# Kernel optimization log

Measured on AMD Instinct MI355X. Metric: run time of the kernel, lower is better.

Reference implementation:

```python
import jax, jax.numpy as jnp
import numpy as np

H = 2048   # hidden_size
E = 4096   # intermediate_size
N = 16     # ssm_state_size
K = 4      # conv_kernel
R = 128    # time_step_rank
B_SZ = 2
L = 2048


def setup_inputs() -> dict:
    key = jax.random.key(0)
    ks = jax.random.split(key, 9)
    s = lambda fan: 1.0 / np.sqrt(fan)
    hidden_states = jax.random.normal(ks[0], (B_SZ, L, H), dtype=jnp.float32)
    in_proj_w = jax.random.normal(ks[1], (2 * E, H), dtype=jnp.float32) * s(H)
    conv_w = jax.random.normal(ks[2], (E, 1, K), dtype=jnp.float32) * s(K)
    conv_b = jax.random.normal(ks[3], (E,), dtype=jnp.float32) * 0.01
    x_proj_w = jax.random.normal(ks[4], (R + 2 * N, E), dtype=jnp.float32) * s(E)
    dt_proj_w = jax.random.normal(ks[5], (E, R), dtype=jnp.float32) * s(R)
    dt_proj_b = jax.random.normal(ks[6], (E,), dtype=jnp.float32) * 0.01
    A_log = jnp.log(jnp.broadcast_to(jnp.arange(1, N + 1, dtype=jnp.float32)[None, :], (E, N)))
    D = jnp.ones((E,), dtype=jnp.float32)
    out_proj_w = jax.random.normal(ks[7], (H, E), dtype=jnp.float32) * s(E)
    return {
        "hidden_states": hidden_states,
        "in_proj_w": in_proj_w,
        "conv_w": conv_w,
        "conv_b": conv_b,
        "x_proj_w": x_proj_w,
        "dt_proj_w": dt_proj_w,
        "dt_proj_b": dt_proj_b,
        "A_log": A_log,
        "D": D,
        "out_proj_w": out_proj_w,
    }


def _mamba_fwd(hidden_states, in_proj_w, conv_w, conv_b, x_proj_w,
               dt_proj_w, dt_proj_b, A_log, D, out_proj_w):
    # in_proj -> [B, L, 2E] -> transpose -> [B, 2E, L] -> chunk
    proj = jnp.einsum('blh,eh->ble', hidden_states, in_proj_w)
    proj = jnp.transpose(proj, (0, 2, 1))              # [B, 2E, L]
    u, gate = jnp.split(proj, 2, axis=1)               # each [B, E, L]

    # causal depthwise conv1d (pad K-1 left), then silu
    x = jax.lax.conv_general_dilated(
        u, conv_w, window_strides=(1,), padding=[(K - 1, 0)],
        dimension_numbers=('NCH', 'OIH', 'NCH'), feature_group_count=E)
    x = jax.nn.silu(x + conv_b[None, :, None])          # [B, E, L]

    # x_proj -> dt, B, C
    x_bl = jnp.transpose(x, (0, 2, 1))                  # [B, L, E]
    x_dbl = jnp.einsum('ble,re->blr', x_bl, x_proj_w)   # [B, L, R+2N]
    dt_low, Bmat, Cmat = jnp.split(x_dbl, [R, R + N], axis=-1)
    dt = jax.nn.softplus(jnp.einsum('blr,er->ble', dt_low, dt_proj_w) + dt_proj_b)  # [B, L, E]

    A = -jnp.exp(A_log)                                 # [E, N]

    # selective scan over time; carry state [B, E, N]
    def step(s, inp):
        dt_t, u_t, B_t, C_t = inp                       # [B,E],[B,E],[B,N],[B,N]
        dA = jnp.exp(dt_t[..., None] * A[None])         # [B, E, N]
        s = s * dA + (dt_t * u_t)[..., None] * B_t[:, None, :]
        y_t = jnp.einsum('ben,bn->be', s, C_t)
        return s, y_t

    xs = (jnp.transpose(dt, (1, 0, 2)),                 # [L, B, E]
          jnp.transpose(x, (2, 0, 1)),                  # [L, B, E]
          jnp.transpose(Bmat, (1, 0, 2)),               # [L, B, N]
          jnp.transpose(Cmat, (1, 0, 2)))               # [L, B, N]
    s0 = jnp.zeros((hidden_states.shape[0], E, N), dtype=jnp.float32)
    _, ys = jax.lax.scan(step, s0, xs)                  # ys: [L, B, E]

    y = jnp.transpose(ys, (1, 2, 0))                    # [B, E, L]
    y = y + x * D[None, :, None]
    y = y * jax.nn.silu(gate)
    out = jnp.einsum('bel,he->blh', y, out_proj_w)      # [B, L, H]
    return out


def reference(hidden_states, in_proj_w, conv_w, conv_b, x_proj_w,
              dt_proj_w, dt_proj_b, A_log, D, out_proj_w):
    return _mamba_fwd(hidden_states, in_proj_w, conv_w, conv_b, x_proj_w,
                      dt_proj_w, dt_proj_b, A_log, D, out_proj_w)
```

## Files before the change

kernel.cpp:

```cpp
#include <hip/hip_runtime.h>
#include <math.h>

#define Hd 2048
#define Ed 4096
#define Nssm 16
#define Rrank 128
#define Bb 2
#define Ll 2048
#define Mrows (Bb*Ll)
#define XDBL_C 160
#define Cc 64
#define Tc (Ll/Cc)

typedef unsigned short u16;
typedef short bf16x8 __attribute__((ext_vector_type(8)));
typedef float f32x4 __attribute__((ext_vector_type(4)));
typedef u16 us4 __attribute__((ext_vector_type(4)));
typedef u16 us8 __attribute__((ext_vector_type(8)));

__device__ __forceinline__ u16 f2bf(float f) {
    unsigned u = __float_as_uint(f);
    u += 0x7FFFu + ((u >> 16) & 1u);
    return (u16)(u >> 16);
}
__device__ __forceinline__ float bf2f(u16 h) {
    return __uint_as_float((unsigned)h << 16);
}
__device__ __forceinline__ float fexp(float x)  { return __expf(x); }
__device__ __forceinline__ float fsig(float x)  { return __builtin_amdgcn_rcpf(1.f + __expf(-x)); }
__device__ __forceinline__ float fsoftplus(float z) {
    return fmaxf(z, 0.f) + __logf(1.f + __expf(-fabsf(z)));
}

__device__ __forceinline__ void stage_tile(const char* g, int ldbytes, char* lds, int tid)
{
#pragma unroll
    for (int q = 0; q < 4; ++q) {
        int idx = q * 256 + tid;
        int row = idx >> 3;
        int cb  = (idx & 7) << 4;
        int sb  = cb ^ ((row & 7) << 4);
        __builtin_amdgcn_global_load_lds(
            (const __attribute__((address_space(1))) void*)(g + (size_t)row * ldbytes + sb),
            (__attribute__((address_space(3))) void*)(lds + (size_t)idx * 16),
            16, 0, 0);
    }
}

__device__ __forceinline__ void stage_half(const char* g, int ldbytes, char* lds, int tid)
{
#pragma unroll
    for (int q = 0; q < 2; ++q) {
        int idx = q * 512 + tid;
        int row = idx >> 3;
        int cb  = (idx & 7) << 4;
        int sb  = cb ^ ((row & 7) << 4);
        __builtin_amdgcn_global_load_lds(
            (const __attribute__((address_space(1))) void*)(g + (size_t)row * ldbytes + sb),
            (__attribute__((address_space(3))) void*)(lds + (size_t)idx * 16),
            16, 0, 0);
    }
}

template<int NKT, int CBF16>
__global__ __launch_bounds__(512, 2)
void gemm_3buf(const u16* __restrict__ A, const u16* __restrict__ Bw,
               void* __restrict__ Cp, int ld, int ldc)
{
    __shared__ __align__(16) char lds[147456];
    const int tid = threadIdx.x;
    const int bm = blockIdx.y * 256;
    const int bn = blockIdx.x * 128;
    const int lane = tid & 63;
    const int wv = tid >> 6;
    const int wm = wv >> 1;
    const int wn = wv & 1;
    const int lr = lane & 15, kg = lane >> 4;

    f32x4 acc[4][4];
#pragma unroll
    for (int f = 0; f < 4; ++f)
#pragma unroll
        for (int g = 0; g < 4; ++g) acc[f][g] = (f32x4){0.f, 0.f, 0.f, 0.f};

    bf16x8 av[4][2], bv[2][2];

#define BUFA(b) (lds + (b) * 49152)
#define BUFB(b) (lds + (b) * 49152 + 32768)
#define STAGE_A3(t, b) { \
    stage_half((const char*)A + ((size_t)(bm)       * ld + (t)*64) * 2, ld*2, BUFA(b), tid); \
    stage_half((const char*)A + ((size_t)(bm + 128) * ld + (t)*64) * 2, ld*2, BUFA(b) + 16384, tid); }
#define STAGE_B3(t, b) \
    stage_half((const char*)Bw + ((size_t)(bn)      * ld + (t)*64) * 2, ld*2, BUFB(b), tid)
#define READ_A3(b) { const char* p_ = BUFA(b); \
    _Pragma("unroll") for (int f = 0; f < 4; ++f) { \
        int row = wm*64 + f*16 + lr; int sw = (row & 7) << 4; \
        const char* rb = p_ + row * 128; \
        av[f][0] = *(const bf16x8*)(rb + ((kg*16) ^ sw)); \
        av[f][1] = *(const bf16x8*)(rb + ((64 + kg*16) ^ sw)); } }
#define READ_B3(b, u) { const char* p_ = BUFB(b); \
    _Pragma("unroll") for (int g = 0; g < 2; ++g) { \
        int row = wn*64 + (u)*32 + g*16 + lr; int sw = (row & 7) << 4; \
        const char* rb = p_ + row * 128; \
        bv[g][0] = *(const bf16x8*)(rb + ((kg*16) ^ sw)); \
        bv[g][1] = *(const bf16x8*)(rb + ((64 + kg*16) ^ sw)); } }
#define QUAD3(u) { \
    _Pragma("unroll") for (int f = 0; f < 4; ++f) \
    _Pragma("unroll") for (int g = 0; g < 2; ++g) { \
        acc[f][(u)*2+g] = __builtin_amdgcn_mfma_f32_16x16x32_bf16(av[f][0], bv[g][0], acc[f][(u)*2+g], 0, 0, 0); \
        acc[f][(u)*2+g] = __builtin_amdgcn_mfma_f32_16x16x32_bf16(av[f][1], bv[g][1], acc[f][(u)*2+g], 0, 0, 0); } }
#define BAR __builtin_amdgcn_s_barrier()
#define VMW(n) { asm volatile("s_waitcnt vmcnt(" #n ")" ::: "memory"); __builtin_amdgcn_sched_barrier(0); }

    STAGE_A3(0, 0); STAGE_B3(0, 0);
    STAGE_A3(1, 1); STAGE_B3(1, 1);
    VMW(6);
    BAR;

    int bc = 0;
    for (int t = 0; t < NKT; ++t) {
        int b2 = bc + 2; if (b2 >= 3) b2 -= 3;
        READ_A3(bc); READ_B3(bc, 0);
        if (t + 2 < NKT) STAGE_A3(t + 2, b2);
        BAR; __builtin_amdgcn_s_setprio(1); QUAD3(0); __builtin_amdgcn_s_setprio(0); BAR;
        READ_B3(bc, 1);
        if (t + 2 < NKT) STAGE_B3(t + 2, b2);
        BAR; __builtin_amdgcn_s_setprio(1); QUAD3(1); __builtin_amdgcn_s_setprio(0);
        if (t + 2 < NKT) { VMW(6); } else if (t + 1 < NKT) { VMW(0); }
        BAR;
        bc = (bc + 1 == 3) ? 0 : bc + 1;
    }

#pragma unroll
    for (int f = 0; f < 4; ++f) {
        int rbase = bm + wm * 64 + f * 16 + kg * 4;
#pragma unroll
        for (int g = 0; g < 4; ++g) {
            int col = bn + wn * 64 + g * 16 + lr;
#pragma unroll
            for (int r = 0; r < 4; ++r) {
                float v = acc[f][g][r];
                if (CBF16) ((u16*)Cp)[(size_t)(rbase + r) * ldc + col] = f2bf(v);
                else       ((float*)Cp)[(size_t)(rbase + r) * ldc + col] = v;
            }
        }
    }
#undef BUFA
#undef BUFB
#undef STAGE_A3
#undef STAGE_B3
#undef READ_A3
#undef READ_B3
#undef QUAD3
#undef BAR
#undef VMW
}

template<int EPI, int CBF16>
__global__ __launch_bounds__(256)
void gemm_bf16(const u16* __restrict__ A, const u16* __restrict__ Bw,
               void* __restrict__ Cp, const float* __restrict__ bias,
               int Nv, int Ksub, int lda, int ldb, int ldc, size_t zstride)
{
    __shared__ __align__(16) char lds[32768];
    char* ldsA = lds;
    char* ldsB = lds + 16384;
    const int tid = threadIdx.x;
    const int bm = blockIdx.y * 128;
    const int bn = blockIdx.x * 128;
    const int lane = tid & 63, wv = tid >> 6;
    const int wr = (wv >> 1) * 64, wc = (wv & 1) * 64;
    const int lr = lane & 15, kg = lane >> 4;
    const int kbeg = blockIdx.z * Ksub;

    f32x4 acc[4][4];
#pragma unroll
    for (int m = 0; m < 4; ++m)
#pragma unroll
        for (int n = 0; n < 4; ++n) acc[m][n] = (f32x4){0.f, 0.f, 0.f, 0.f};

    for (int k0 = kbeg; k0 < kbeg + Ksub; k0 += 64) {
        stage_tile((const char*)A  + ((size_t)bm * lda + k0) * 2, lda * 2, ldsA, tid);
        stage_tile((const char*)Bw + ((size_t)bn * ldb + k0) * 2, ldb * 2, ldsB, tid);
        __syncthreads();
#pragma unroll
        for (int kk = 0; kk < 2; ++kk) {
            const int bc = kk * 64 + kg * 16;
            bf16x8 bfr[4], af[4];
#pragma unroll
            for (int n = 0; n < 4; ++n) {
                int row = wc + n * 16 + lr;
                bfr[n] = *(const bf16x8*)(ldsB + row * 128 + (bc ^ ((row & 7) << 4)));
            }
#pragma unroll
            for (int m = 0; m < 4; ++m) {
                int row = wr + m * 16 + lr;
                af[m] = *(const bf16x8*)(ldsA + row * 128 + (bc ^ ((row & 7) << 4)));
            }
#pragma unroll
            for (int m = 0; m < 4; ++m)
#pragma unroll
                for (int n = 0; n < 4; ++n)
                    acc[m][n] = __builtin_amdgcn_mfma_f32_16x16x32_bf16(af[m], bfr[n], acc[m][n], 0, 0, 0);
        }
        __syncthreads();
    }

    if (zstride) Cp = (void*)((float*)Cp + (size_t)blockIdx.z * zstride);

#pragma unroll
    for (int m = 0; m < 4; ++m) {
        int rbase = bm + wr + m * 16 + kg * 4;
#pragma unroll
        for (int n = 0; n < 4; ++n) {
            int col = bn + wc + n * 16 + lr;
            if (col < Nv) {
#pragma unroll
                for (int r = 0; r < 4; ++r) {
                    float v = acc[m][n][r];
                    if (EPI == 1) v = fsoftplus(v + bias[col]);
                    if (CBF16) ((u16*)Cp)[(size_t)(rbase + r) * ldc + col] = f2bf(v);
                    else       ((float*)Cp)[(size_t)(rbase + r) * ldc + col] = v;
                }
            }
        }
    }
}

__global__ __launch_bounds__(256)
void reduce_cast(const float* __restrict__ part, float* __restrict__ outf,
                 u16* __restrict__ outb, int cnt, size_t stride, int total)
{
    int i = blockIdx.x * 256 + threadIdx.x;
    if (i < total) {
        float v = 0.f;
        for (int z = 0; z < cnt; z++) v += part[(size_t)z * stride + i];
        outf[i] = v;
        outb[i] = f2bf(v);
    }
}

__global__ __launch_bounds__(256)
void cast_w(const float* __restrict__ s, u16* __restrict__ d, int n)
{
    int i = (blockIdx.x * 256 + threadIdx.x) * 8;
    if (i >= n) return;
    float4 a = *(const float4*)(s + i);
    float4 b = *(const float4*)(s + i + 4);
    us8 o;
    o[0] = f2bf(a.x); o[1] = f2bf(a.y); o[2] = f2bf(a.z); o[3] = f2bf(a.w);
    o[4] = f2bf(b.x); o[5] = f2bf(b.y); o[6] = f2bf(b.z); o[7] = f2bf(b.w);
    *(us8*)(d + i) = o;
}

__global__ __launch_bounds__(256)
void cast_wx(const float* __restrict__ s, u16* __restrict__ d)
{
    int i4 = (blockIdx.x * 256 + threadIdx.x) * 4;
    int row = i4 >> 12;
    us4 o = (us4){0, 0, 0, 0};
    if (row < XDBL_C) {
        float4 v = *(const float4*)(s + i4);
        o[0] = f2bf(v.x); o[1] = f2bf(v.y); o[2] = f2bf(v.z); o[3] = f2bf(v.w);
    }
    *(us4*)(d + i4) = o;
}

__global__ __launch_bounds__(256)
void conv_silu_bf(const u16* __restrict__ proj, const float* __restrict__ cw,
                  const float* __restrict__ cb, u16* __restrict__ x)
{
    const int e  = blockIdx.x * 256 + threadIdx.x;
    const int t0 = blockIdx.y * 32;
    const int bz = blockIdx.z;
    const float4 w4 = *(const float4*)(cw + (size_t)e * 4);
    const float bias = cb[e];
    const size_t base = (size_t)bz * Ll * (2 * Ed) + e;

    float u0 = 0.f, u1 = 0.f, u2 = 0.f;
    if (t0 >= 3) {
        u0 = bf2f(proj[base + (size_t)(t0 - 3) * (2 * Ed)]);
        u1 = bf2f(proj[base + (size_t)(t0 - 2) * (2 * Ed)]);
        u2 = bf2f(proj[base + (size_t)(t0 - 1) * (2 * Ed)]);
    }
    size_t xo = ((size_t)(bz * Ll + t0)) * Ed + e;
#pragma unroll 4
    for (int t = t0; t < t0 + 32; ++t) {
        float u3 = bf2f(proj[base + (size_t)t * (2 * Ed)]);
        float acc = bias;
        acc = fmaf(w4.x, u0, acc);
        acc = fmaf(w4.y, u1, acc);
        acc = fmaf(w4.z, u2, acc);
        acc = fmaf(w4.w, u3, acc);
        float sx = acc * fsig(acc);
        x[xo] = f2bf(sx);
        xo += Ed;
        u0 = u1; u1 = u2; u2 = u3;
    }
}

__global__ __launch_bounds__(256)
void scan_part1(const u16* __restrict__ proj, const u16* __restrict__ x,
                const float* __restrict__ xdbl, const float* __restrict__ Alog,
                float* __restrict__ S, float* __restrict__ sumdt)
{
    const int e = blockIdx.x * 256 + threadIdx.x;
    const int c = blockIdx.y;
    const int b = blockIdx.z;

    float Ae[Nssm];
#pragma unroll
    for (int n = 0; n < Nssm; n++) Ae[n] = -fexp(Alog[(size_t)e * Nssm + n]);

    float s[Nssm];
#pragma unroll
    for (int n = 0; n < Nssm; n++) s[n] = 0.f;
    float sdt = 0.f;

    const size_t row0 = (size_t)b * Ll + (size_t)c * Tc;
    for (int t = 0; t < Tc; ++t) {
        size_t r = row0 + t;
        float dtv = bf2f(proj[r * (2 * Ed) + e]);
        float uv  = bf2f(x[r * Ed + e]);
        const float* p = xdbl + r * XDBL_C + Rrank;
        float du = dtv * uv;
        sdt += dtv;
#pragma unroll
        for (int n = 0; n < Nssm; n++)
            s[n] = fmaf(s[n], fexp(dtv * Ae[n]), du * p[n]);
    }

    float* sp = S + ((((size_t)b * Cc + c) * Ed + e) * Nssm);
#pragma unroll
    for (int n = 0; n < Nssm; n += 4)
        *(float4*)(sp + n) = make_float4(s[n], s[n+1], s[n+2], s[n+3]);
    sumdt[((size_t)b * Cc + c) * Ed + e] = sdt;
}

__global__ __launch_bounds__(256)
void scan_mid(float* __restrict__ S, const float* __restrict__ sumdt,
              const float* __restrict__ Alog)
{
    const int idx = blockIdx.x * 256 + threadIdx.x;
    const int n = idx & (Nssm - 1);
    const int e = (idx >> 4) & (Ed - 1);
    const int b = idx >> 16;
    const float Ae = -fexp(Alog[(size_t)e * Nssm + n]);
    float carry = 0.f;
    for (int c = 0; c < Cc; ++c) {
        size_t off = (((size_t)b * Cc + c) * Ed + e) * Nssm + n;
        float sl = S[off];
        float P  = fexp(Ae * sumdt[((size_t)b * Cc + c) * Ed + e]);
        S[off] = carry;
        carry = fmaf(P, carry, sl);
    }
}

__global__ __launch_bounds__(256)
void scan_part2(const u16* __restrict__ proj, u16* __restrict__ x,
                const float* __restrict__ xdbl, const float* __restrict__ Alog,
                const float* __restrict__ Dvec, const float* __restrict__ S)
{
    const int e = blockIdx.x * 256 + threadIdx.x;
    const int c = blockIdx.y;
    const int b = blockIdx.z;

    float Ae[Nssm];
#pragma unroll
    for (int n = 0; n < Nssm; n++) Ae[n] = -fexp(Alog[(size_t)e * Nssm + n]);
    const float Dv = Dvec[e];

    float s[Nssm];
    const float* sp = S + ((((size_t)b * Cc + c) * Ed + e) * Nssm);
#pragma unroll
    for (int n = 0; n < Nssm; n += 4) {
        float4 v = *(const float4*)(sp + n);
        s[n] = v.x; s[n+1] = v.y; s[n+2] = v.z; s[n+3] = v.w;
    }

    const size_t row0 = (size_t)b * Ll + (size_t)c * Tc;
    for (int t = 0; t < Tc; ++t) {
        size_t r = row0 + t;
        float dtv = bf2f(proj[r * (2 * Ed) + e]);
        float uv  = bf2f(x[r * Ed + e]);
        float gv  = bf2f(proj[r * (2 * Ed) + Ed + e]);
        const float* p = xdbl + r * XDBL_C + Rrank;
        float du = dtv * uv;
        float y = 0.f;
#pragma unroll
        for (int n = 0; n < Nssm; n++) {
            float dA = fexp(dtv * Ae[n]);
            s[n] = fmaf(s[n], dA, du * p[n]);
            y = fmaf(s[n], p[Nssm + n], y);
        }
        float yv = (y + uv * Dv) * (gv * fsig(gv));
        x[r * Ed + e] = f2bf(yv);
    }
}

extern "C" void kernel_launch(void* const* d_in, const int* in_sizes, int n_in,
                              void* d_out, int out_size, void* d_ws, size_t ws_size,
                              hipStream_t stream) {
    const float* hs    = (const float*)d_in[0];
    const float* w_in  = (const float*)d_in[1];
    const float* cw    = (const float*)d_in[2];
    const float* cb    = (const float*)d_in[3];
    const float* w_x   = (const float*)d_in[4];
    const float* w_dt  = (const float*)d_in[5];
    const float* b_dt  = (const float*)d_in[6];
    const float* Alog  = (const float*)d_in[7];
    const float* Dvec  = (const float*)d_in[8];
    const float* w_out = (const float*)d_in[9];
    float* out = (float*)d_out;

    char* w = (char*)d_ws;
    u16*  proj_bf  = (u16*)w;
    u16*  x_bf     = (u16*)(w + 67108864);
    u16*  w_in_bf  = (u16*)(w + 100663296);
    u16*  w_out_bf = (u16*)(w + 134217728);
    u16*  hs_bf    = (u16*)(w + 150994944);
    u16*  w_x_bf   = (u16*)(w + 167772160);
    u16*  w_dt_bf  = (u16*)(w + 169869312);
    float* xdbl    = (float*)(w + 170917888);
    u16*  xdbl_bf  = (u16*)(w + 173539328);
    float* part    = (float*)(w + 174850048);
    float* sumdt   = (float*)(w + 185335808);
    float* S       = (float*)(w + 187432960);

    dim3 blk(256);

    cast_w<<<dim3(8192), blk, 0, stream>>>(w_in, w_in_bf, 2 * Ed * Hd);
    cast_w<<<dim3(4096), blk, 0, stream>>>(w_out, w_out_bf, Hd * Ed);
    cast_w<<<dim3(256),  blk, 0, stream>>>(w_dt, w_dt_bf, Ed * Rrank);
    cast_wx<<<dim3(1024), blk, 0, stream>>>(w_x, w_x_bf);
    cast_w<<<dim3(4096), blk, 0, stream>>>(hs, hs_bf, Mrows * Hd);

    gemm_3buf<Hd / 64, 1><<<dim3(2 * Ed / 128, Mrows / 256), dim3(512), 0, stream>>>(
        hs_bf, w_in_bf, proj_bf, Hd, 2 * Ed);

    conv_silu_bf<<<dim3(Ed / 256, Ll / 32, Bb), blk, 0, stream>>>(proj_bf, cw, cb, x_bf);

    gemm_bf16<0, 0><<<dim3(2, 32, 4), blk, 0, stream>>>(
        x_bf, w_x_bf, part, nullptr, XDBL_C, Ed / 4, Ed, Ed, XDBL_C,
        (size_t)Mrows * XDBL_C);
    reduce_cast<<<dim3((Mrows * XDBL_C + 255) / 256), blk, 0, stream>>>(
        part, xdbl, xdbl_bf, 4, (size_t)Mrows * XDBL_C, Mrows * XDBL_C);

    gemm_bf16<1, 1><<<dim3(32, 32, 1), blk, 0, stream>>>(
        xdbl_bf, w_dt_bf, proj_bf, b_dt, Ed, Rrank, XDBL_C, Rrank, 2 * Ed, 0);

    scan_part1<<<dim3(Ed / 256, Cc, Bb), blk, 0, stream>>>(
        proj_bf, x_bf, xdbl, Alog, S, sumdt);
    scan_mid<<<dim3(Bb * Ed * Nssm / 256), blk, 0, stream>>>(S, sumdt, Alog);
    scan_part2<<<dim3(Ed / 256, Cc, Bb), blk, 0, stream>>>(
        proj_bf, x_bf, xdbl, Alog, Dvec, S);

    gemm_3buf<Ed / 64, 0><<<dim3(Hd / 128, Mrows / 256), dim3(512), 0, stream>>>(
        x_bf, w_out_bf, out, Ed, Hd);
}
```

Measured before the change: 418.9 us.

## Replace in_proj GEMM with 256x256-tile eight-phase pipelined kernel

Swaps the 256x128-tile triple-buffered in_proj GEMM for a new 256x256-tile kernel. It double-buffers A and B half-tiles in LDS and interleaves half-tile global-to-LDS loads with MFMA quadrants over eight barrier-separated phases, raising wave priority around the MFMA bursts. The larger tile increases operand reuse per block and halves the grid in N. In exchange it holds more accumulator registers per thread and adds many barriers with hand-tuned vmcnt waits that must match the load order exactly.

```diff
diff --git a/kernel.cpp b/kernel.cpp
--- a/kernel.cpp
+++ b/kernel.cpp
@@ -60,6 +60,118 @@
             (__attribute__((address_space(3))) void*)(lds + (size_t)idx * 16),
             16, 0, 0);
     }
+}
+
+#define NK8  32
+#define NI8  16
+
+__global__ __launch_bounds__(512, 2)
+void gemm_8ph_inproj(const u16* __restrict__ A, const u16* __restrict__ Bw,
+                     u16* __restrict__ C)
+{
+    __shared__ __align__(16) char lds[131072];
+    const int tid = threadIdx.x;
+    const int bm = blockIdx.y * 256;
+    const int bn = blockIdx.x * 256;
+    const int lane = tid & 63;
+    const int wv = tid >> 6;
+    const int wm = wv >> 2;
+    const int wn = wv & 3;
+    const int lr = lane & 15, kg = lane >> 4;
+
+    f32x4 acc[8][4];
+#pragma unroll
+    for (int m = 0; m < 8; ++m)
+#pragma unroll
+        for (int n = 0; n < 4; ++n) acc[m][n] = (f32x4){0.f, 0.f, 0.f, 0.f};
+
+    bf16x8 av[4][2], bv0[2][2], bv1[2][2];
+
+#define ASLOT(d, h) (lds + ((d)*2 + (h)) * 16384)
+#define BSLOT(d, h) (lds + 65536 + ((d)*2 + (h)) * 16384)
+#define STAGE_AH(t, h) stage_half((const char*)A  + ((size_t)(bm + (h)*128) * Hd + (t)*64) * 2, Hd*2, ASLOT((t)&1, h), tid)
+#define STAGE_BH(t, h) stage_half((const char*)Bw + ((size_t)(bn + (h)*128) * Hd + (t)*64) * 2, Hd*2, BSLOT((t)&1, h), tid)
+
+#define READ_A(d, s) { \
+    const char* slot_ = ASLOT(d, wm); \
+    _Pragma("unroll") for (int f = 0; f < 4; ++f) { \
+        int row = (s)*64 + f*16 + lr; int sw = (row & 7) << 4; \
+        const char* rb = slot_ + row * 128; \
+        av[f][0] = *(const bf16x8*)(rb + ((kg*16) ^ sw)); \
+        av[f][1] = *(const bf16x8*)(rb + ((64 + kg*16) ^ sw)); } }
+#define READ_B(d, u, bvX) { \
+    const char* slot_ = BSLOT(d, (wn >> 1)); \
+    _Pragma("unroll") for (int g2 = 0; g2 < 2; ++g2) { \
+        int row = (wn & 1)*64 + (u)*32 + g2*16 + lr; int sw = (row & 7) << 4; \
+        const char* rb = slot_ + row * 128; \
+        bvX[g2][0] = *(const bf16x8*)(rb + ((kg*16) ^ sw)); \
+        bvX[g2][1] = *(const bf16x8*)(rb + ((64 + kg*16) ^ sw)); } }
+#define QUAD(s, u, bvX) { \
+    _Pragma("unroll") for (int f = 0; f < 4; ++f) \
+    _Pragma("unroll") for (int g2 = 0; g2 < 2; ++g2) { \
+        acc[(s)*4+f][(u)*2+g2] = __builtin_amdgcn_mfma_f32_16x16x32_bf16(av[f][0], bvX[g2][0], acc[(s)*4+f][(u)*2+g2], 0, 0, 0); \
+        acc[(s)*4+f][(u)*2+g2] = __builtin_amdgcn_mfma_f32_16x16x32_bf16(av[f][1], bvX[g2][1], acc[(s)*4+f][(u)*2+g2], 0, 0, 0); } }
+
+#define BAR __builtin_amdgcn_s_barrier()
+#define PRIO1 __builtin_amdgcn_s_setprio(1)
+#define PRIO0 __builtin_amdgcn_s_setprio(0)
+#define VMW(n) { asm volatile("s_waitcnt vmcnt(" #n ")" ::: "memory"); __builtin_amdgcn_sched_barrier(0); }
+
+    STAGE_BH(0, 0); STAGE_BH(0, 1); STAGE_AH(0, 0); STAGE_AH(0, 1);
+    STAGE_BH(1, 0); STAGE_BH(1, 1);
+    VMW(4);
+    BAR;
+
+    for (int i = 0; i < NI8; ++i) {
+        const int o = 2*i + 1, t2 = 2*i + 2, t3 = 2*i + 3;
+        READ_A(0, 0); READ_B(0, 0, bv0);
+        STAGE_AH(o, 0);
+        BAR; PRIO1; QUAD(0, 0, bv0); PRIO0; BAR;
+        READ_B(0, 1, bv1);
+        STAGE_AH(o, 1);
+        BAR; PRIO1; QUAD(0, 1, bv1); PRIO0; VMW(6); BAR;
+        READ_A(0, 1);
+        if (t2 < NK8) STAGE_BH(t2, 0);
+        BAR; PRIO1; QUAD(1, 0, bv0); PRIO0; BAR;
+        if (t2 < NK8) STAGE_BH(t2, 1);
+        BAR; PRIO1; QUAD(1, 1, bv1); PRIO0;
+        if (i == NI8 - 1) { VMW(0); } else { VMW(6); }
+        BAR;
+        READ_A(1, 0); READ_B(1, 0, bv0);
+        if (t2 < NK8) STAGE_AH(t2, 0);
+        BAR; PRIO1; QUAD(0, 0, bv0); PRIO0; BAR;
+        READ_B(1, 1, bv1);
+        if (t2 < NK8) STAGE_AH(t2, 1);
+        BAR; PRIO1; QUAD(0, 1, bv1); PRIO0; VMW(6); BAR;
+        READ_A(1, 1);
+        if (t3 < NK8) STAGE_BH(t3, 0);
+        BAR; PRIO1; QUAD(1, 0, bv0); PRIO0; BAR;
+        if (t3 < NK8) STAGE_BH(t3, 1);
+        BAR; PRIO1; QUAD(1, 1, bv1); PRIO0; VMW(6); BAR;
+    }
+
+#pragma unroll
+    for (int m = 0; m < 8; ++m) {
+        int rbase = bm + wm * 128 + m * 16 + kg * 4;
+#pragma unroll
+        for (int n = 0; n < 4; ++n) {
+            int col = bn + wn * 64 + n * 16 + lr;
+#pragma unroll
+            for (int r = 0; r < 4; ++r)
+                C[(size_t)(rbase + r) * (2 * Ed) + col] = f2bf(acc[m][n][r]);
+        }
+    }
+#undef ASLOT
+#undef BSLOT
+#undef STAGE_AH
+#undef STAGE_BH
+#undef READ_A
+#undef READ_B
+#undef QUAD
+#undef BAR
+#undef PRIO1
+#undef PRIO0
+#undef VMW
 }
 
 template<int NKT, int CBF16>
@@ -435,8 +547,8 @@
     cast_wx<<<dim3(1024), blk, 0, stream>>>(w_x, w_x_bf);
     cast_w<<<dim3(4096), blk, 0, stream>>>(hs, hs_bf, Mrows * Hd);
 
-    gemm_3buf<Hd / 64, 1><<<dim3(2 * Ed / 128, Mrows / 256), dim3(512), 0, stream>>>(
-        hs_bf, w_in_bf, proj_bf, Hd, 2 * Ed);
+    gemm_8ph_inproj<<<dim3(2 * Ed / 256, Mrows / 256), dim3(512), 0, stream>>>(
+        hs_bf, w_in_bf, proj_bf);
 
     conv_silu_bf<<<dim3(Ed / 256, Ll / 32, Bb), blk, 0, stream>>>(proj_bf, cw, cb, x_bf);
 
```

Result: faster. 402.8 us (-3.8%).
